# Kernel optimization log

Measured on AMD Instinct MI355X. Metric: run time of the kernel, lower is better.

The kernel has to match this reference:

```python
import jax, jax.numpy as jnp
import numpy as np

B, N, D = 8, 1024, 768
H = 12
HD = D // H
LN_EPS = 1e-5
EPS = 1e-8


def setup_inputs() -> dict:
    key = jax.random.key(0)
    ks = jax.random.split(key, 16)
    s = 0.02
    return {
        "x": jax.random.normal(ks[0], (B, N, D), jnp.float32),
        "low_freq_feat": jax.random.normal(ks[1], (B, N, D), jnp.float32),
        "high_freq_feat": jax.random.normal(ks[2], (B, N, D), jnp.float32),
        "W_qkv_id": jax.random.normal(ks[3], (D, 3 * D), jnp.float32) * s,
        "W_qkv_attr": jax.random.normal(ks[4], (D, 3 * D), jnp.float32) * s,
        "W_fg_id": jax.random.normal(ks[5], (D, D), jnp.float32) * s,
        "b_fg_id": jnp.zeros((D,), jnp.float32),
        "W_fg_attr": jax.random.normal(ks[6], (D, D), jnp.float32) * s,
        "b_fg_attr": jnp.zeros((D,), jnp.float32),
        "W_proj_id": jax.random.normal(ks[7], (D, D), jnp.float32) * s,
        "b_proj_id": jnp.zeros((D,), jnp.float32),
        "W_proj_attr": jax.random.normal(ks[8], (D, D), jnp.float32) * s,
        "b_proj_attr": jnp.zeros((D,), jnp.float32),
        "ln_id_g": jnp.ones((D,), jnp.float32),
        "ln_id_b": jnp.zeros((D,), jnp.float32),
        "ln_attr_g": jnp.ones((D,), jnp.float32),
        "ln_attr_b": jnp.zeros((D,), jnp.float32),
        "ortho_temperature": jnp.float32(1.0),
        "freq_guide_strength": jnp.float32(0.3),
    }


def _layernorm(x, g, b):
    mu = x.mean(-1, keepdims=True)
    var = ((x - mu) ** 2).mean(-1, keepdims=True)
    return (x - mu) * jax.lax.rsqrt(var + LN_EPS) * g + b


def reference(x, low_freq_feat, high_freq_feat,
              W_qkv_id, W_qkv_attr,
              W_fg_id, b_fg_id, W_fg_attr, b_fg_attr,
              W_proj_id, b_proj_id, W_proj_attr, b_proj_attr,
              ln_id_g, ln_id_b, ln_attr_g, ln_attr_b,
              ortho_temperature, freq_guide_strength):
    b, n, d = x.shape
    scale = HD ** -0.5

    def split_qkv(t):
        t = t.reshape(b, n, 3, H, HD).transpose(2, 0, 3, 1, 4)
        return t[0], t[1], t[2]

    q_id, k_id, v_id = split_qkv(x @ W_qkv_id)
    q_at, k_at, v_at = split_qkv(x @ W_qkv_attr)

    fs = jax.nn.sigmoid(freq_guide_strength)
    low_g = (low_freq_feat @ W_fg_id + b_fg_id).reshape(b, n, H, HD).transpose(0, 2, 1, 3)
    high_g = (high_freq_feat @ W_fg_attr + b_fg_attr).reshape(b, n, H, HD).transpose(0, 2, 1, 3)
    v_id = v_id + fs * low_g
    v_at = v_at + fs * high_g

    def soft_attn(q, k):
        a = jnp.clip(jnp.einsum('bhnd,bhmd->bhnm', q, k) * scale, -20.0, 20.0)
        return jax.nn.softmax(a, axis=-1)

    attn_id = soft_attn(q_id, k_id)
    attn_at = soft_attn(q_at, k_at)

    # soft orthogonal mask (same mask for both branches)
    overlap = ((attn_id + EPS) * (attn_at + EPS)).sum(-1, keepdims=True)
    temp = jnp.clip(ortho_temperature, 0.1, 5.0)
    mask = jax.nn.sigmoid(-overlap * temp)

    def mask_renorm(a):
        m = a * mask
        m = m / (m.sum(-1, keepdims=True) + EPS)
        return jnp.where(jnp.isnan(m), jnp.zeros_like(m), m)

    attn_id = mask_renorm(attn_id)
    attn_at = mask_renorm(attn_at)

    def branch_out(a, v, W, bias, g, beta):
        o = jnp.einsum('bhnm,bhmd->bhnd', a, v).transpose(0, 2, 1, 3).reshape(b, n, d)
        return _layernorm(o @ W + bias, g, beta)

    id_features = branch_out(attn_id, v_id, W_proj_id, b_proj_id, ln_id_g, ln_id_b)
    attr_features = branch_out(attn_at, v_at, W_proj_attr, b_proj_attr, ln_attr_g, ln_attr_b)
    return (id_features, attr_features)
```

## Files before the change

kernel.cpp:

```cpp
#include <hip/hip_runtime.h>
#include <stdint.h>


typedef __attribute__((ext_vector_type(8))) _Float16 f16x8;
typedef __attribute__((ext_vector_type(4))) _Float16 f16x4;
typedef __attribute__((ext_vector_type(4))) float    f32x4;

__device__ __forceinline__ void g2l16(const void* g, void* l) {
  __builtin_amdgcn_global_load_lds(
      (const __attribute__((address_space(1))) void*)g,
      (__attribute__((address_space(3))) void*)l, 16, 0, 0);
}

#define BARX()   asm volatile("s_barrier" ::: "memory")
#define WAITV0() asm volatile("s_waitcnt vmcnt(0)" ::: "memory")
#define LGKM0()  asm volatile("s_waitcnt lgkmcnt(0)" ::: "memory")
#define SB0()    __builtin_amdgcn_sched_barrier(0)

#define MFMA12(NB)                                                            \
  __builtin_amdgcn_s_setprio(1);                                              \
  _Pragma("unroll")                                                           \
  for (int mt = 0; mt < 4; mt++)                                              \
    _Pragma("unroll")                                                         \
    for (int i = 0; i < 3; i++)                                               \
      acc[mt][(NB) + i] = SWAP                                                \
          ? __builtin_amdgcn_mfma_f32_16x16x32_f16(b[i], a[mt],               \
                                                   acc[mt][(NB) + i], 0, 0, 0)\
          : __builtin_amdgcn_mfma_f32_16x16x32_f16(a[mt], b[i],               \
                                                   acc[mt][(NB) + i], 0, 0, 0);\
  __builtin_amdgcn_s_setprio(0);

template <bool SWAP>
__device__ __forceinline__ void gemm192(const _Float16* __restrict__ A,
                                        const _Float16* __restrict__ Bt,
                                        int K, int m0, int n0,
                                        _Float16* As, _Float16* Bs,
                                        f32x4 (&acc)[4][6]) {
  const int tid = threadIdx.x;
  const int lane = tid & 63, w = tid >> 6;
  const int wm = (w >> 1) * 64, wn = (w & 1) * 96;
  const int l15 = lane & 15, quad = lane >> 4;
  const int srow = lane >> 2;
  const int scol = ((lane & 3) ^ ((lane >> 3) & 3)) * 8;
  const int rg = (quad ^ ((l15 >> 1) & 3)) * 8;
  const int rdA = (wm + l15) * 32 + rg;
  const int rdB = (wn + l15) * 32 + rg;
  const int KT = K >> 6;

  const _Float16* gA0 = A + (size_t)(m0 + (w * 2) * 16 + srow) * K + scol;
  const _Float16* gA1 = gA0 + (size_t)16 * K;
  const _Float16* gB[3]; int lB[3];
#pragma unroll
  for (int i = 0; i < 3; i++) {
    int j = w * 3 + i, hb = j / 12, cb = j % 12;
    gB[i] = Bt + (size_t)(n0 + cb * 16 + srow) * K + hb * 32 + scol;
    lB[i] = hb * 6144 + cb * 512;
  }

  auto stageA = [&](int t) {
    const int kc = t * 64;
    _Float16* Ab = As + (t & 1) * 16384 + w * 1024;
    g2l16(gA0 + kc,      Ab);
    g2l16(gA0 + kc + 32, Ab + 8192);
    g2l16(gA1 + kc,      Ab + 512);
    g2l16(gA1 + kc + 32, Ab + 8704);
  };
  auto stageB = [&](int t) {
    const int kc = t * 64;
    _Float16* Bb = Bs + (t & 1) * 12288;
#pragma unroll
    for (int i = 0; i < 3; i++) g2l16(gB[i] + kc, Bb + lB[i]);
  };

#pragma unroll
  for (int mt = 0; mt < 4; mt++)
#pragma unroll
    for (int nt = 0; nt < 6; nt++) acc[mt][nt] = (f32x4){0.f, 0.f, 0.f, 0.f};

  stageA(0); stageB(0);
  WAITV0();
  BARX();

  for (int t = 0; t < KT; t++) {
    const _Float16* as = As + (t & 1) * 16384;
    const _Float16* bs = Bs + (t & 1) * 12288;
    const bool st = (t + 1 < KT);
    f16x8 a[4], b[3];

#pragma unroll
    for (int mt = 0; mt < 4; mt++) a[mt] = *(const f16x8*)(as + rdA + mt * 512);
#pragma unroll
    for (int i = 0; i < 3; i++) b[i] = *(const f16x8*)(bs + rdB + i * 512);
    if (st) stageA(t + 1);
    BARX(); LGKM0(); SB0();
    MFMA12(0);
    SB0();
    BARX();

#pragma unroll
    for (int i = 0; i < 3; i++) b[i] = *(const f16x8*)(bs + rdB + (3 + i) * 512);
    if (st) stageB(t + 1);
    BARX(); LGKM0(); SB0();
    MFMA12(3);
    SB0();
    BARX();

#pragma unroll
    for (int mt = 0; mt < 4; mt++)
      a[mt] = *(const f16x8*)(as + 8192 + rdA + mt * 512);
#pragma unroll
    for (int i = 0; i < 3; i++)
      b[i] = *(const f16x8*)(bs + 6144 + rdB + i * 512);
    BARX(); LGKM0(); SB0();
    MFMA12(0);
    SB0();
    BARX();

#pragma unroll
    for (int i = 0; i < 3; i++)
      b[i] = *(const f16x8*)(bs + 6144 + rdB + (3 + i) * 512);
    BARX(); LGKM0(); SB0();
    MFMA12(3);
    SB0();
    WAITV0();
    BARX();
  }
}

__global__ __launch_bounds__(256) void k_cast3(const float* __restrict__ s0,
                                               const float* __restrict__ s1,
                                               const float* __restrict__ s2,
                                               _Float16* __restrict__ d0,
                                               _Float16* __restrict__ d1,
                                               _Float16* __restrict__ d2) {
  int blk = blockIdx.x;
  const float* s; _Float16* d;
  if (blk < 6144)       { s = s0; d = d0; }
  else if (blk < 12288) { s = s1; d = d1; blk -= 6144; }
  else                  { s = s2; d = d2; blk -= 12288; }
  int i = blk * 256 + threadIdx.x;
  float4 v = ((const float4*)s)[i];
  f16x4 o = {(_Float16)v.x, (_Float16)v.y, (_Float16)v.z, (_Float16)v.w};
  *(f16x4*)(d + (size_t)i * 4) = o;
}

__device__ __forceinline__ void tcast32(const float* __restrict__ src,
                                        _Float16* __restrict__ dst,
                                        int N, int n0, int k0) {
  __shared__ float t[32][33];
  int tr = threadIdx.x >> 5, tc = threadIdx.x & 31;
#pragma unroll
  for (int i = 0; i < 4; i++) {
    int r = tr + i * 8;
    t[r][tc] = src[(size_t)(k0 + r) * N + n0 + tc];
  }
  __syncthreads();
#pragma unroll
  for (int i = 0; i < 4; i++) {
    int r = tr + i * 8;
    dst[(size_t)(n0 + r) * 768 + k0 + tc] = (_Float16)t[tc][r];
  }
}

__global__ __launch_bounds__(256) void k_tcast_all(const float* __restrict__ Wq0,
                                                   const float* __restrict__ Wq1,
                                                   const float* __restrict__ W0,
                                                   const float* __restrict__ W1,
                                                   const float* __restrict__ W2,
                                                   const float* __restrict__ W3,
                                                   _Float16* __restrict__ Dq,
                                                   _Float16* __restrict__ D0,
                                                   _Float16* __restrict__ D1,
                                                   _Float16* __restrict__ D2,
                                                   _Float16* __restrict__ D3) {
  int blk = blockIdx.x;
  if (blk < 3456) {
    int half = blk / 1728, rem = blk % 1728;
    int xx = rem % 72, yy = rem / 72;
    tcast32(half ? Wq1 : Wq0, Dq + (size_t)half * 2304 * 768, 2304, xx * 32, yy * 32);
  } else {
    blk -= 3456;
    int q = blk / 576, rem = blk % 576;
    int xx = rem % 24, yy = rem / 24;
    const float* src; _Float16* d;
    if (q == 0)      { src = W0; d = D0; }
    else if (q == 1) { src = W1; d = D1; }
    else if (q == 2) { src = W2; d = D2; }
    else             { src = W3; d = D3; }
    tcast32(src, d, 768, xx * 32, yy * 32);
  }
}

__global__ __launch_bounds__(512, 2) void k_gemm_qkv(const _Float16* __restrict__ A,
                                                     const _Float16* __restrict__ Bt,
                                                     _Float16* __restrict__ Qb,
                                                     _Float16* __restrict__ Kb,
                                                     _Float16* __restrict__ Vtb) {
  __shared__ alignas(16) _Float16 As[32768], Bs[24576];
  f32x4 acc[4][6];
  int m0 = blockIdx.y * 256, n0 = blockIdx.x * 192;
  int br = n0 / 2304;
  int three = (n0 - br * 2304) / 768;
  int lane = threadIdx.x & 63, w = threadIdx.x >> 6;
  int wm = (w >> 1) * 64, wn = (w & 1) * 96, l15 = lane & 15, quad = lane >> 4;

  if (three == 2) {
    gemm192<false>(A, Bt, 768, m0, n0, As, Bs, acc);
#pragma unroll
    for (int mt = 0; mt < 4; mt++)
#pragma unroll
      for (int nt = 0; nt < 6; nt++) {
        int n = n0 + wn + nt * 16 + l15;
        int c = n - br * 2304 - 1536;
        int h = c >> 6, hd = c & 63;
        int m = m0 + wm + mt * 16 + quad * 4;
        int b = m >> 10, tok = m & 1023;
        size_t head = (size_t)(br * 96 + b * 12 + h);
        f32x4 v = acc[mt][nt];
        f16x4 o;
#pragma unroll
        for (int r = 0; r < 4; r++) o[r] = (_Float16)v[r];
        *(f16x4*)(Vtb + (head * 64 + hd) * 1024 + tok) = o;
      }
  } else {
    gemm192<true>(A, Bt, 768, m0, n0, As, Bs, acc);
    float qscl = (three == 0) ? 0.125f * 1.44269504f : 1.0f;
    _Float16* dst = (three == 0) ? Qb : Kb;
#pragma unroll
    for (int mt = 0; mt < 4; mt++)
#pragma unroll
      for (int nt = 0; nt < 6; nt++) {
        int m = m0 + wm + mt * 16 + l15;
        int n = n0 + wn + nt * 16 + quad * 4;
        int c = n - br * 2304 - three * 768;
        int h = c >> 6, hd = c & 63;
        int b = m >> 10, tok = m & 1023;
        size_t head = (size_t)(br * 96 + b * 12 + h);
        f32x4 v = acc[mt][nt];
        f16x4 o;
#pragma unroll
        for (int r = 0; r < 4; r++) o[r] = (_Float16)(v[r] * qscl);
        *(f16x4*)(dst + (head * 1024 + tok) * 64 + hd) = o;
      }
  }
}

__global__ __launch_bounds__(512, 2) void k_gemm_fgadd(const _Float16* __restrict__ Alo,
                                                       const _Float16* __restrict__ Ahi,
                                                       const _Float16* __restrict__ Bid,
                                                       const _Float16* __restrict__ Bat,
                                                       const float* __restrict__ bid,
                                                       const float* __restrict__ bat,
                                                       const float* __restrict__ fgs,
                                                       _Float16* __restrict__ Vtb) {
  __shared__ alignas(16) _Float16 As[32768], Bs[24576];
  f32x4 acc[4][6];
  int br = blockIdx.x >> 2;
  int n0 = (blockIdx.x & 3) * 192, m0 = blockIdx.y * 256;
  const _Float16* A = br ? Ahi : Alo;
  const _Float16* Bt = br ? Bat : Bid;
  const float* bias = br ? bat : bid;
  gemm192<false>(A, Bt, 768, m0, n0, As, Bs, acc);
  float fs = 1.f / (1.f + __expf(-fgs[0]));
  int lane = threadIdx.x & 63, w = threadIdx.x >> 6;
  int wm = (w >> 1) * 64, wn = (w & 1) * 96, l15 = lane & 15, quad = lane >> 4;
#pragma unroll
  for (int mt = 0; mt < 4; mt++)
#pragma unroll
    for (int nt = 0; nt < 6; nt++) {
      int c = n0 + wn + nt * 16 + l15;
      int h = c >> 6, hd = c & 63;
      int m = m0 + wm + mt * 16 + quad * 4;
      int b = m >> 10, tok = m & 1023;
      size_t head = (size_t)(br * 96 + b * 12 + h);
      float bv = bias[c];
      f32x4 v = acc[mt][nt];
      _Float16* p = Vtb + (head * 64 + hd) * 1024 + tok;
      f16x4 old = *(const f16x4*)p;
      f16x4 o;
#pragma unroll
      for (int r = 0; r < 4; r++)
        o[r] = (_Float16)((float)old[r] + fs * (v[r] + bv));
      *(f16x4*)p = o;
    }
}

__global__ __launch_bounds__(256, 3) void k_attn(const _Float16* __restrict__ Qb,
                                                 const _Float16* __restrict__ Kb,
                                                 const _Float16* __restrict__ Vtb,
                                                 _Float16* __restrict__ Ob) {
  __shared__ alignas(16) _Float16 Qs[128 * 64];
  __shared__ alignas(16) _Float16 Ks[128 * 64];
  __shared__ alignas(16) _Float16 Vts[64 * 128];
  int hl = blockIdx.x;
  int br = hl / 96, bh = hl % 96;
  int qbase = blockIdx.y * 128;
  const _Float16* Qh = Qb + (size_t)hl * 65536;
  const _Float16* Kh = Kb + (size_t)hl * 65536;
  const _Float16* Vth = Vtb + (size_t)hl * 65536;
  int lane = threadIdx.x & 63, w = threadIdx.x >> 6;
  int l15 = lane & 15, quad = lane >> 4;
  const int key7 = l15 & 7;

  {
    int rr = lane >> 3, sg = (lane & 7) ^ rr;
#pragma unroll
    for (int i = 0; i < 4; i++) {
      int c = w * 4 + i;
      g2l16(Qh + (size_t)(qbase + c * 8 + rr) * 64 + sg * 8, Qs + c * 512);
    }
  }
  auto stage_kv = [&](int n0) {
    int rr8 = lane >> 3, sg8 = ((lane & 7) ^ rr8) * 8;
    int rr16 = lane >> 4;
#pragma unroll
    for (int i = 0; i < 4; i++) {
      int c = w * 4 + i;
      g2l16(Kh + (size_t)(n0 + c * 8 + rr8) * 64 + sg8, Ks + c * 512);
      int vrow = c * 4 + rr16;
      int sg16 = ((lane & 15) ^ (vrow & 15)) * 8;
      g2l16(Vth + (size_t)vrow * 1024 + n0 + sg16, Vts + c * 512);
    }
  };
  stage_kv(0);

  f32x4 o[2][4];
#pragma unroll
  for (int qg = 0; qg < 2; qg++)
#pragma unroll
    for (int i = 0; i < 4; i++) o[qg][i] = (f32x4){0.f, 0.f, 0.f, 0.f};
  float rs0 = 0.f, rs1 = 0.f;
  f16x8 bq[2][2];
  const f32x4 zero = (f32x4){0.f, 0.f, 0.f, 0.f};
  const int g0 = (quad ^ key7) * 8, g1 = ((4 + quad) ^ key7) * 8;

  for (int kt = 0; kt < 8; kt++) {
    __syncthreads();
    if (kt == 0) {
#pragma unroll
      for (int qg = 0; qg < 2; qg++) {
        bq[qg][0] = *(const f16x8*)(Qs + (w * 32 + qg * 16 + l15) * 64 + g0);
        bq[qg][1] = *(const f16x8*)(Qs + (w * 32 + qg * 16 + l15) * 64 + g1);
      }
    }
    f32x4 c0, c1;
    {
      f16x8 a0 = *(const f16x8*)(Ks + l15 * 64 + g0);
      f16x8 a1 = *(const f16x8*)(Ks + l15 * 64 + g1);
      c0 = __builtin_amdgcn_mfma_f32_16x16x32_f16(a0, bq[0][0], zero, 0, 0, 0);
      c0 = __builtin_amdgcn_mfma_f32_16x16x32_f16(a1, bq[0][1], c0, 0, 0, 0);
      c1 = __builtin_amdgcn_mfma_f32_16x16x32_f16(a0, bq[1][0], zero, 0, 0, 0);
      c1 = __builtin_amdgcn_mfma_f32_16x16x32_f16(a1, bq[1][1], c1, 0, 0, 0);
    }
#pragma unroll
    for (int nt = 0; nt < 8; nt++) {
      f32x4 n0_, n1_;
      if (nt < 7) {
        f16x8 a0 = *(const f16x8*)(Ks + ((nt + 1) * 16 + l15) * 64 + g0);
        f16x8 a1 = *(const f16x8*)(Ks + ((nt + 1) * 16 + l15) * 64 + g1);
        n0_ = __builtin_amdgcn_mfma_f32_16x16x32_f16(a0, bq[0][0], zero, 0, 0, 0);
        n0_ = __builtin_amdgcn_mfma_f32_16x16x32_f16(a1, bq[0][1], n0_, 0, 0, 0);
        n1_ = __builtin_amdgcn_mfma_f32_16x16x32_f16(a0, bq[1][0], zero, 0, 0, 0);
        n1_ = __builtin_amdgcn_mfma_f32_16x16x32_f16(a1, bq[1][1], n1_, 0, 0, 0);
      }
      f16x4 pt0, pt1;
#pragma unroll
      for (int r = 0; r < 4; r++) {
        float p = __builtin_amdgcn_exp2f(c0[r]);
        rs0 += p; pt0[r] = (_Float16)p;
      }
#pragma unroll
      for (int r = 0; r < 4; r++) {
        float p = __builtin_amdgcn_exp2f(c1[r]);
        rs1 += p; pt1[r] = (_Float16)p;
      }
#pragma unroll
      for (int hdt = 0; hdt < 4; hdt++) {
        int g = ((2 * nt + (quad >> 1)) ^ l15) * 8 + (quad & 1) * 4;
        f16x4 av = *(const f16x4*)(Vts + (hdt * 16 + l15) * 128 + g);
        o[0][hdt] = __builtin_amdgcn_mfma_f32_16x16x16f16(av, pt0, o[0][hdt], 0, 0, 0);
        o[1][hdt] = __builtin_amdgcn_mfma_f32_16x16x16f16(av, pt1, o[1][hdt], 0, 0, 0);
      }
      if (nt < 7) { c0 = n0_; c1 = n1_; }
    }
    __syncthreads();
    if (kt < 7) stage_kv((kt + 1) * 128);
  }
  int b = bh / 12, h = bh % 12;
#pragma unroll
  for (int qg = 0; qg < 2; qg++) {
    float l = qg ? rs1 : rs0;
    l += __shfl_xor(l, 16);
    l += __shfl_xor(l, 32);
    float inv = 1.f / l;
    size_t rowb = ((size_t)br * 8192 + b * 1024 + qbase + w * 32 + qg * 16 + l15) * 768 +
                  h * 64;
#pragma unroll
    for (int hdt = 0; hdt < 4; hdt++) {
      f16x4 u;
#pragma unroll
      for (int r = 0; r < 4; r++) u[r] = (_Float16)(o[qg][hdt][r] * inv);
      *(f16x4*)(Ob + rowb + hdt * 16 + quad * 4) = u;
    }
  }
}

__global__ __launch_bounds__(512, 2) void k_gemm_proj2(const _Float16* __restrict__ Aid,
                                                       const _Float16* __restrict__ Aat,
                                                       const _Float16* __restrict__ Bid,
                                                       const _Float16* __restrict__ Bat,
                                                       _Float16* __restrict__ Yid,
                                                       _Float16* __restrict__ Yat) {
  __shared__ alignas(16) _Float16 As[32768], Bs[24576];
  f32x4 acc[4][6];
  int half = blockIdx.x >> 2;
  int n0 = (blockIdx.x & 3) * 192, m0 = blockIdx.y * 256;
  const _Float16* A = half ? Aat : Aid;
  const _Float16* Bt = half ? Bat : Bid;
  _Float16* Y = half ? Yat : Yid;
  gemm192<true>(A, Bt, 768, m0, n0, As, Bs, acc);
  int lane = threadIdx.x & 63, w = threadIdx.x >> 6;
  int wm = (w >> 1) * 64, wn = (w & 1) * 96, l15 = lane & 15, quad = lane >> 4;
#pragma unroll
  for (int mt = 0; mt < 4; mt++)
#pragma unroll
    for (int nt = 0; nt < 6; nt++) {
      int m = m0 + wm + mt * 16 + l15;
      int n = n0 + wn + nt * 16 + quad * 4;
      f32x4 v = acc[mt][nt];
      f16x4 o;
#pragma unroll
      for (int r = 0; r < 4; r++) o[r] = (_Float16)v[r];
      *(f16x4*)(Y + (size_t)m * 768 + n) = o;
    }
}

__global__ __launch_bounds__(256) void k_ln(const _Float16* __restrict__ Yid,
                                            const _Float16* __restrict__ Yat,
                                            const float* __restrict__ bp_id,
                                            const float* __restrict__ bp_at,
                                            const float* __restrict__ g_id,
                                            const float* __restrict__ be_id,
                                            const float* __restrict__ g_at,
                                            const float* __restrict__ be_at,
                                            float* __restrict__ out) {
  int w = threadIdx.x >> 6, lane = threadIdx.x & 63;
  int r = blockIdx.x * 4 + w;
  int br = r >> 13, m = r & 8191;
  const _Float16* Y = br ? Yat : Yid;
  const float* bp = br ? bp_at : bp_id;
  const float* g = br ? g_at : g_id;
  const float* be = br ? be_at : be_id;
  float v[12], sum = 0.f, sq = 0.f;
#pragma unroll
  for (int j = 0; j < 3; j++) {
    int c = j * 256 + lane * 4;
    f16x4 y = *(const f16x4*)(Y + (size_t)m * 768 + c);
    float4 bv = *(const float4*)(bp + c);
#pragma unroll
    for (int r2 = 0; r2 < 4; r2++) {
      float t = (float)y[r2] + ((const float*)&bv)[r2];
      v[j * 4 + r2] = t; sum += t; sq += t * t;
    }
  }
#pragma unroll
  for (int d = 1; d < 64; d <<= 1) { sum += __shfl_xor(sum, d); sq += __shfl_xor(sq, d); }
  float mu = sum * (1.f / 768.f);
  float var = sq * (1.f / 768.f) - mu * mu;
  float rstd = rsqrtf(var + 1e-5f);
  float* op = out + (size_t)br * 6291456 + (size_t)m * 768;
#pragma unroll
  for (int j = 0; j < 3; j++) {
    int c = j * 256 + lane * 4;
    float4 gv = *(const float4*)(g + c);
    float4 bev = *(const float4*)(be + c);
    float4 ov;
#pragma unroll
    for (int r2 = 0; r2 < 4; r2++)
      ((float*)&ov)[r2] = (v[j * 4 + r2] - mu) * rstd * ((const float*)&gv)[r2] +
                          ((const float*)&bev)[r2];
    *(float4*)(op + c) = ov;
  }
}

extern "C" void kernel_launch(void* const* d_in, const int* in_sizes, int n_in,
                              void* d_out, int out_size, void* d_ws, size_t ws_size,
                              hipStream_t stream) {
  const float* x       = (const float*)d_in[0];
  const float* lowf    = (const float*)d_in[1];
  const float* highf   = (const float*)d_in[2];
  const float* Wqkv_id = (const float*)d_in[3];
  const float* Wqkv_at = (const float*)d_in[4];
  const float* Wfg_id  = (const float*)d_in[5];
  const float* bfg_id  = (const float*)d_in[6];
  const float* Wfg_at  = (const float*)d_in[7];
  const float* bfg_at  = (const float*)d_in[8];
  const float* Wpr_id  = (const float*)d_in[9];
  const float* bpr_id  = (const float*)d_in[10];
  const float* Wpr_at  = (const float*)d_in[11];
  const float* bpr_at  = (const float*)d_in[12];
  const float* g_id    = (const float*)d_in[13];
  const float* be_id   = (const float*)d_in[14];
  const float* g_at    = (const float*)d_in[15];
  const float* be_at   = (const float*)d_in[16];
  const float* fgs     = (const float*)d_in[18];

  char* ws = (char*)d_ws;
  _Float16* x_f    = (_Float16*)(ws + 0);
  _Float16* low_f  = (_Float16*)(ws + 12582912);
  _Float16* high_f = (_Float16*)(ws + 25165824);
  _Float16* wqkvt  = (_Float16*)(ws + 37748736);
  _Float16* wfgidt = (_Float16*)(ws + 44826624);
  _Float16* wfgatt = (_Float16*)(ws + 46006272);
  _Float16* wpridt = (_Float16*)(ws + 47185920);
  _Float16* wpratt = (_Float16*)(ws + 48365568);
  _Float16* Qb     = (_Float16*)(ws + 74711040);
  _Float16* Kb     = (_Float16*)(ws + 99876864);
  _Float16* Vtb    = (_Float16*)(ws + 125042688);
  _Float16* Ob     = (_Float16*)(ws + 150208512);
  _Float16* Y_id   = (_Float16*)(ws + 0);
  _Float16* Y_at   = (_Float16*)(ws + 49545216);

  k_cast3<<<18432, 256, 0, stream>>>(x, lowf, highf, x_f, low_f, high_f);
  k_tcast_all<<<5760, 256, 0, stream>>>(Wqkv_id, Wqkv_at, Wfg_id, Wfg_at, Wpr_id, Wpr_at,
                                        wqkvt, wfgidt, wfgatt, wpridt, wpratt);
  k_gemm_qkv<<<dim3(24, 32), 512, 0, stream>>>(x_f, wqkvt, Qb, Kb, Vtb);
  k_gemm_fgadd<<<dim3(8, 32), 512, 0, stream>>>(low_f, high_f, wfgidt, wfgatt,
                                                bfg_id, bfg_at, fgs, Vtb);
  k_attn<<<dim3(192, 8), 256, 0, stream>>>(Qb, Kb, Vtb, Ob);
  k_gemm_proj2<<<dim3(8, 32), 512, 0, stream>>>(Ob, Ob + 6291456, wpridt, wpratt,
                                                Y_id, Y_at);
  k_ln<<<4096, 256, 0, stream>>>(Y_id, Y_at, bpr_id, bpr_at, g_id, be_id, g_at, be_at,
                                 (float*)d_out);
}
```

Baseline: 395.7 us.

## Fuse frequency-guide GEMM into V projection via concatenated K and merge cast kernels

The V-part of the QKV GEMM now runs a K=1536 reduction over [x | sigmoid(fs)*low/high] against [Wqkv_v ; W_fg], so the guide projection accumulates in the same tile. This removes the separate fgadd GEMM kernel, its read-modify-write of Vtb, and one launch. The sigmoid scale is folded into the fp16 cast of low/high, and that cast is merged with the weight transpose-cast into one prep kernel. V blocks now do twice the K-loop of Q/K blocks, which creates load imbalance inside the QKV grid, and scaling before the fp16 cast changes rounding slightly.

```diff
diff --git a/kernel.cpp b/kernel.cpp
--- a/kernel.cpp
+++ b/kernel.cpp
@@ -31,9 +31,11 @@
   __builtin_amdgcn_s_setprio(0);
 
 template <bool SWAP>
-__device__ __forceinline__ void gemm192(const _Float16* __restrict__ A,
-                                        const _Float16* __restrict__ Bt,
-                                        int K, int m0, int n0,
+__device__ __forceinline__ void gemm192(const _Float16* __restrict__ A0,
+                                        const _Float16* __restrict__ A1,
+                                        const _Float16* __restrict__ B0,
+                                        const _Float16* __restrict__ B1,
+                                        int nb0, int nb1, int m0, int KT,
                                         _Float16* As, _Float16* Bs,
                                         f32x4 (&acc)[4][6]) {
   const int tid = threadIdx.x;
@@ -45,31 +47,40 @@
   const int rg = (quad ^ ((l15 >> 1) & 3)) * 8;
   const int rdA = (wm + l15) * 32 + rg;
   const int rdB = (wn + l15) * 32 + rg;
-  const int KT = K >> 6;
-
-  const _Float16* gA0 = A + (size_t)(m0 + (w * 2) * 16 + srow) * K + scol;
-  const _Float16* gA1 = gA0 + (size_t)16 * K;
-  const _Float16* gB[3]; int lB[3];
+
+  const _Float16* gA0a = A0 + (size_t)(m0 + (w * 2) * 16 + srow) * 768 + scol;
+  const _Float16* gA1a = gA0a + (size_t)16 * 768;
+  const _Float16* gA0b = A1 + (size_t)(m0 + (w * 2) * 16 + srow) * 768 + scol;
+  const _Float16* gA1b = gA0b + (size_t)16 * 768;
+  const _Float16* gBa[3]; const _Float16* gBb[3]; int lB[3];
 #pragma unroll
   for (int i = 0; i < 3; i++) {
     int j = w * 3 + i, hb = j / 12, cb = j % 12;
-    gB[i] = Bt + (size_t)(n0 + cb * 16 + srow) * K + hb * 32 + scol;
+    gBa[i] = B0 + (size_t)(nb0 + cb * 16 + srow) * 768 + hb * 32 + scol;
+    gBb[i] = B1 + (size_t)(nb1 + cb * 16 + srow) * 768 + hb * 32 + scol;
     lB[i] = hb * 6144 + cb * 512;
   }
 
   auto stageA = [&](int t) {
-    const int kc = t * 64;
+    const bool s = t >= 12;
+    const int kc = (s ? t - 12 : t) * 64;
+    const _Float16* a0 = s ? gA0b : gA0a;
+    const _Float16* a1 = s ? gA1b : gA1a;
     _Float16* Ab = As + (t & 1) * 16384 + w * 1024;
-    g2l16(gA0 + kc,      Ab);
-    g2l16(gA0 + kc + 32, Ab + 8192);
-    g2l16(gA1 + kc,      Ab + 512);
-    g2l16(gA1 + kc + 32, Ab + 8704);
+    g2l16(a0 + kc,      Ab);
+    g2l16(a0 + kc + 32, Ab + 8192);
+    g2l16(a1 + kc,      Ab + 512);
+    g2l16(a1 + kc + 32, Ab + 8704);
   };
   auto stageB = [&](int t) {
-    const int kc = t * 64;
+    const bool s = t >= 12;
+    const int kc = (s ? t - 12 : t) * 64;
     _Float16* Bb = Bs + (t & 1) * 12288;
 #pragma unroll
-    for (int i = 0; i < 3; i++) g2l16(gB[i] + kc, Bb + lB[i]);
+    for (int i = 0; i < 3; i++) {
+      const _Float16* p = s ? gBb[i] : gBa[i];
+      g2l16(p + kc, Bb + lB[i]);
+    }
   };
 
 #pragma unroll
@@ -127,23 +138,6 @@
   }
 }
 
-__global__ __launch_bounds__(256) void k_cast3(const float* __restrict__ s0,
-                                               const float* __restrict__ s1,
-                                               const float* __restrict__ s2,
-                                               _Float16* __restrict__ d0,
-                                               _Float16* __restrict__ d1,
-                                               _Float16* __restrict__ d2) {
-  int blk = blockIdx.x;
-  const float* s; _Float16* d;
-  if (blk < 6144)       { s = s0; d = d0; }
-  else if (blk < 12288) { s = s1; d = d1; blk -= 6144; }
-  else                  { s = s2; d = d2; blk -= 12288; }
-  int i = blk * 256 + threadIdx.x;
-  float4 v = ((const float4*)s)[i];
-  f16x4 o = {(_Float16)v.x, (_Float16)v.y, (_Float16)v.z, (_Float16)v.w};
-  *(f16x4*)(d + (size_t)i * 4) = o;
-}
-
 __device__ __forceinline__ void tcast32(const float* __restrict__ src,
                                         _Float16* __restrict__ dst,
                                         int N, int n0, int k0) {
@@ -162,18 +156,41 @@
   }
 }
 
-__global__ __launch_bounds__(256) void k_tcast_all(const float* __restrict__ Wq0,
-                                                   const float* __restrict__ Wq1,
-                                                   const float* __restrict__ W0,
-                                                   const float* __restrict__ W1,
-                                                   const float* __restrict__ W2,
-                                                   const float* __restrict__ W3,
-                                                   _Float16* __restrict__ Dq,
-                                                   _Float16* __restrict__ D0,
-                                                   _Float16* __restrict__ D1,
-                                                   _Float16* __restrict__ D2,
-                                                   _Float16* __restrict__ D3) {
+__global__ __launch_bounds__(256) void k_pre(const float* __restrict__ x,
+                                             const float* __restrict__ lo,
+                                             const float* __restrict__ hi,
+                                             const float* __restrict__ fgs,
+                                             const float* __restrict__ Wq0,
+                                             const float* __restrict__ Wq1,
+                                             const float* __restrict__ W0,
+                                             const float* __restrict__ W1,
+                                             const float* __restrict__ W2,
+                                             const float* __restrict__ W3,
+                                             _Float16* __restrict__ x_f,
+                                             _Float16* __restrict__ low_f,
+                                             _Float16* __restrict__ high_f,
+                                             _Float16* __restrict__ Dq,
+                                             _Float16* __restrict__ D0,
+                                             _Float16* __restrict__ D1,
+                                             _Float16* __restrict__ D2,
+                                             _Float16* __restrict__ D3) {
   int blk = blockIdx.x;
+  if (blk < 18432) {
+    float scale = 1.f;
+    const float* s; _Float16* d;
+    if (blk < 6144)       { s = x;  d = x_f; }
+    else if (blk < 12288) { s = lo; d = low_f;  blk -= 6144;
+                            scale = 1.f / (1.f + __expf(-fgs[0])); }
+    else                  { s = hi; d = high_f; blk -= 12288;
+                            scale = 1.f / (1.f + __expf(-fgs[0])); }
+    int i = blk * 256 + threadIdx.x;
+    float4 v = ((const float4*)s)[i];
+    f16x4 o = {(_Float16)(v.x * scale), (_Float16)(v.y * scale),
+               (_Float16)(v.z * scale), (_Float16)(v.w * scale)};
+    *(f16x4*)(d + (size_t)i * 4) = o;
+    return;
+  }
+  blk -= 18432;
   if (blk < 3456) {
     int half = blk / 1728, rem = blk % 1728;
     int xx = rem % 72, yy = rem / 72;
@@ -191,39 +208,51 @@
   }
 }
 
-__global__ __launch_bounds__(512, 2) void k_gemm_qkv(const _Float16* __restrict__ A,
-                                                     const _Float16* __restrict__ Bt,
+__global__ __launch_bounds__(512, 2) void k_gemm_qkv(const _Float16* __restrict__ x_f,
+                                                     const _Float16* __restrict__ low_f,
+                                                     const _Float16* __restrict__ high_f,
+                                                     const _Float16* __restrict__ wqkvt,
+                                                     const _Float16* __restrict__ wfgid,
+                                                     const _Float16* __restrict__ wfgat,
+                                                     const float* __restrict__ bfg_id,
+                                                     const float* __restrict__ bfg_at,
+                                                     const float* __restrict__ fgs,
                                                      _Float16* __restrict__ Qb,
                                                      _Float16* __restrict__ Kb,
                                                      _Float16* __restrict__ Vtb) {
   __shared__ alignas(16) _Float16 As[32768], Bs[24576];
   f32x4 acc[4][6];
-  int m0 = blockIdx.y * 256, n0 = blockIdx.x * 192;
-  int br = n0 / 2304;
-  int three = (n0 - br * 2304) / 768;
+  int bx = blockIdx.x, br = bx / 12, idx = bx % 12;
+  int three = idx >> 2, sub = idx & 3;
+  int m0 = blockIdx.y * 256;
+  int n0abs = br * 2304 + three * 768 + sub * 192;
   int lane = threadIdx.x & 63, w = threadIdx.x >> 6;
   int wm = (w >> 1) * 64, wn = (w & 1) * 96, l15 = lane & 15, quad = lane >> 4;
 
   if (three == 2) {
-    gemm192<false>(A, Bt, 768, m0, n0, As, Bs, acc);
+    const _Float16* A1 = br ? high_f : low_f;
+    const _Float16* B1 = br ? wfgat : wfgid;
+    gemm192<false>(x_f, A1, wqkvt, B1, n0abs, sub * 192, m0, 24, As, Bs, acc);
+    float fs = 1.f / (1.f + __expf(-fgs[0]));
+    const float* bias = br ? bfg_at : bfg_id;
 #pragma unroll
     for (int mt = 0; mt < 4; mt++)
 #pragma unroll
       for (int nt = 0; nt < 6; nt++) {
-        int n = n0 + wn + nt * 16 + l15;
-        int c = n - br * 2304 - 1536;
+        int c = sub * 192 + wn + nt * 16 + l15;
         int h = c >> 6, hd = c & 63;
         int m = m0 + wm + mt * 16 + quad * 4;
         int b = m >> 10, tok = m & 1023;
         size_t head = (size_t)(br * 96 + b * 12 + h);
+        float bv = fs * bias[c];
         f32x4 v = acc[mt][nt];
         f16x4 o;
 #pragma unroll
-        for (int r = 0; r < 4; r++) o[r] = (_Float16)v[r];
+        for (int r = 0; r < 4; r++) o[r] = (_Float16)(v[r] + bv);
         *(f16x4*)(Vtb + (head * 64 + hd) * 1024 + tok) = o;
       }
   } else {
-    gemm192<true>(A, Bt, 768, m0, n0, As, Bs, acc);
+    gemm192<true>(x_f, x_f, wqkvt, wqkvt, n0abs, n0abs, m0, 12, As, Bs, acc);
     float qscl = (three == 0) ? 0.125f * 1.44269504f : 1.0f;
     _Float16* dst = (three == 0) ? Qb : Kb;
 #pragma unroll
@@ -231,8 +260,7 @@
 #pragma unroll
       for (int nt = 0; nt < 6; nt++) {
         int m = m0 + wm + mt * 16 + l15;
-        int n = n0 + wn + nt * 16 + quad * 4;
-        int c = n - br * 2304 - three * 768;
+        int c = sub * 192 + wn + nt * 16 + quad * 4;
         int h = c >> 6, hd = c & 63;
         int b = m >> 10, tok = m & 1023;
         size_t head = (size_t)(br * 96 + b * 12 + h);
@@ -243,46 +271,6 @@
         *(f16x4*)(dst + (head * 1024 + tok) * 64 + hd) = o;
       }
   }
-}
-
-__global__ __launch_bounds__(512, 2) void k_gemm_fgadd(const _Float16* __restrict__ Alo,
-                                                       const _Float16* __restrict__ Ahi,
-                                                       const _Float16* __restrict__ Bid,
-                                                       const _Float16* __restrict__ Bat,
-                                                       const float* __restrict__ bid,
-                                                       const float* __restrict__ bat,
-                                                       const float* __restrict__ fgs,
-                                                       _Float16* __restrict__ Vtb) {
-  __shared__ alignas(16) _Float16 As[32768], Bs[24576];
-  f32x4 acc[4][6];
-  int br = blockIdx.x >> 2;
-  int n0 = (blockIdx.x & 3) * 192, m0 = blockIdx.y * 256;
-  const _Float16* A = br ? Ahi : Alo;
-  const _Float16* Bt = br ? Bat : Bid;
-  const float* bias = br ? bat : bid;
-  gemm192<false>(A, Bt, 768, m0, n0, As, Bs, acc);
-  float fs = 1.f / (1.f + __expf(-fgs[0]));
-  int lane = threadIdx.x & 63, w = threadIdx.x >> 6;
-  int wm = (w >> 1) * 64, wn = (w & 1) * 96, l15 = lane & 15, quad = lane >> 4;
-#pragma unroll
-  for (int mt = 0; mt < 4; mt++)
-#pragma unroll
-    for (int nt = 0; nt < 6; nt++) {
-      int c = n0 + wn + nt * 16 + l15;
-      int h = c >> 6, hd = c & 63;
-      int m = m0 + wm + mt * 16 + quad * 4;
-      int b = m >> 10, tok = m & 1023;
-      size_t head = (size_t)(br * 96 + b * 12 + h);
-      float bv = bias[c];
-      f32x4 v = acc[mt][nt];
-      _Float16* p = Vtb + (head * 64 + hd) * 1024 + tok;
-      f16x4 old = *(const f16x4*)p;
-      f16x4 o;
-#pragma unroll
-      for (int r = 0; r < 4; r++)
-        o[r] = (_Float16)((float)old[r] + fs * (v[r] + bv));
-      *(f16x4*)p = o;
-    }
 }
 
 __global__ __launch_bounds__(256, 3) void k_attn(const _Float16* __restrict__ Qb,
@@ -418,7 +406,7 @@
   const _Float16* A = half ? Aat : Aid;
   const _Float16* Bt = half ? Bat : Bid;
   _Float16* Y = half ? Yat : Yid;
-  gemm192<true>(A, Bt, 768, m0, n0, As, Bs, acc);
+  gemm192<true>(A, A, Bt, Bt, n0, n0, m0, 12, As, Bs, acc);
   int lane = threadIdx.x & 63, w = threadIdx.x >> 6;
   int wm = (w >> 1) * 64, wn = (w & 1) * 96, l15 = lane & 15, quad = lane >> 4;
 #pragma unroll
@@ -521,12 +509,13 @@
   _Float16* Y_id   = (_Float16*)(ws + 0);
   _Float16* Y_at   = (_Float16*)(ws + 49545216);
 
-  k_cast3<<<18432, 256, 0, stream>>>(x, lowf, highf, x_f, low_f, high_f);
-  k_tcast_all<<<5760, 256, 0, stream>>>(Wqkv_id, Wqkv_at, Wfg_id, Wfg_at, Wpr_id, Wpr_at,
-                                        wqkvt, wfgidt, wfgatt, wpridt, wpratt);
-  k_gemm_qkv<<<dim3(24, 32), 512, 0, stream>>>(x_f, wqkvt, Qb, Kb, Vtb);
-  k_gemm_fgadd<<<dim3(8, 32), 512, 0, stream>>>(low_f, high_f, wfgidt, wfgatt,
-                                                bfg_id, bfg_at, fgs, Vtb);
+  k_pre<<<24192, 256, 0, stream>>>(x, lowf, highf, fgs,
+                                   Wqkv_id, Wqkv_at, Wfg_id, Wfg_at, Wpr_id, Wpr_at,
+                                   x_f, low_f, high_f,
+                                   wqkvt, wfgidt, wfgatt, wpridt, wpratt);
+  k_gemm_qkv<<<dim3(24, 32), 512, 0, stream>>>(x_f, low_f, high_f, wqkvt,
+                                               wfgidt, wfgatt, bfg_id, bfg_at, fgs,
+                                               Qb, Kb, Vtb);
   k_attn<<<dim3(192, 8), 256, 0, stream>>>(Qb, Kb, Vtb, Ob);
   k_gemm_proj2<<<dim3(8, 32), 512, 0, stream>>>(Ob, Ob + 6291456, wpridt, wpratt,
                                                 Y_id, Y_at);
```

Result: no change. 395.7 us (+0.0%).
